# Kernel optimization log

Measured on AMD Instinct MI355X. Metric: run time of the kernel, lower is better.

## Reference

```python
import jax, jax.numpy as jnp
import numpy as np

B, N, D = 4, 8192, 128
H = 4 * D  # exp_factor * features
EPS = 1e-5


def layer_norm(x):
    # fresh nn.LayerNorm each call -> weight=1, bias=0 (no learned affine)
    mu = jnp.mean(x, axis=-1, keepdims=True)
    var = jnp.var(x, axis=-1, keepdims=True)
    return (x - mu) * jax.lax.rsqrt(var + EPS)


def setup_inputs() -> dict:
    key = jax.random.key(0)
    ks = jax.random.split(key, 8)
    x = jax.random.normal(ks[0], (B, N, D), dtype=jnp.float32)
    adj = jax.random.uniform(ks[1], (N, N), dtype=jnp.float32)
    attn_mask = jnp.ones((1,), dtype=jnp.int32)  # unused (torch masked_fill result discarded)
    pad_mask = jnp.ones((1,), dtype=jnp.int32)   # unused
    # FFN params (torch Linear default init scale ~ 1/sqrt(fan_in))
    w1 = jax.random.normal(ks[2], (D, H), dtype=jnp.float32) / np.sqrt(D)
    b1 = jnp.zeros((H,), dtype=jnp.float32)
    w2 = jax.random.normal(ks[3], (H, D), dtype=jnp.float32) / np.sqrt(H)
    b2 = jnp.zeros((D,), dtype=jnp.float32)
    return {"x": x, "adj": adj, "attn_mask": attn_mask, "pad_mask": pad_mask,
            "w1": w1, "b1": b1, "w2": w2, "b2": b2, "dim": 128}


def reference(x, adj, attn_mask, pad_mask, w1, b1, w2, b2, dim):
    # Sublayer 0: x + InrAwaSA(LN(x))
    h = layer_norm(x)                               # [B,N,D]
    # adj is provided -> scores = dense adj, shared across batch.
    # NOTE: masks are no-ops in the source (masked_fill not in-place).
    prob = jax.nn.softmax(adj, axis=-1)             # [N,N]
    attn_out = jnp.einsum('nm,bmd->bnd', prob, h)   # [B,N,D]
    x1 = x + attn_out
    # Sublayer 1: x1 + FFN(LN(x1))
    h1 = layer_norm(x1)
    ffn = jnp.maximum(h1 @ w1 + b1, 0.0) @ w2 + b2
    return x1 + ffn
```

## Files before the change

### kernel.cpp

```cpp
#include <hip/hip_runtime.h>
#include <hip/hip_bf16.h>

typedef __attribute__((ext_vector_type(8))) short bh8;
typedef __attribute__((ext_vector_type(4))) float fx4;
typedef __attribute__((ext_vector_type(8))) int i32x8;
typedef __attribute__((ext_vector_type(4))) int i32x4;

typedef const __attribute__((address_space(1))) unsigned int* gas_p;
typedef __attribute__((address_space(3))) unsigned int* las_p;

#define MFMA(a, b, c) __builtin_amdgcn_mfma_f32_16x16x32_bf16((a), (b), (c), 0, 0, 0)
#define MFMAS(a, b, c) __builtin_amdgcn_mfma_scale_f32_16x16x128_f8f6f4( \
    (a), (b), (c), 0, 0, 0, 0x7f7f7f7f, 0, 0x7f7f7f7f)

__device__ __forceinline__ unsigned short f2bf(float f) {
  unsigned u = __builtin_bit_cast(unsigned, f);
  u += 0x7fff + ((u >> 16) & 1);
  return (unsigned short)(u >> 16);
}

__device__ __forceinline__ float bflo2f(unsigned u) { return __builtin_bit_cast(float, u << 16); }

__device__ __forceinline__ void gld16(const void* g, void* l) {
  __builtin_amdgcn_global_load_lds((gas_p)g, (las_p)l, 16, 0, 0);
}

__global__ __launch_bounds__(256) void transpose_weights(const float* __restrict__ w1,
                                                         const float* __restrict__ w2,
                                                         unsigned short* __restrict__ w1t,
                                                         unsigned short* __restrict__ w2t) {
  const int tgl = blockIdx.x * 256 + threadIdx.x;
  { const int h = tgl >> 7, d = tgl & 127; w1t[tgl] = f2bf(w1[d * 512 + h]); }
  { const int d = tgl >> 9, h = tgl & 511; w2t[tgl] = f2bf(w2[h * 128 + d]); }
}

__global__ __launch_bounds__(256) void ln1_transpose(const float* __restrict__ x,
                                                     unsigned char* __restrict__ ht) {
  const int t = threadIdx.x, lane = t & 63, w = t >> 6;
  const int mt = blockIdx.x, b = blockIdx.y;
  __shared__ unsigned short tile[128 * 64];
  const float* xb = x + ((size_t)b * 8192 + (size_t)mt * 64) * 128;
  for (int it = 0; it < 16; ++it) {
    const int r = w * 16 + it;
    const float2 v = *(const float2*)(xb + r * 128 + lane * 2);
    float s = v.x + v.y, s2 = v.x * v.x + v.y * v.y;
    #pragma unroll
    for (int o = 1; o < 64; o <<= 1) { s += __shfl_xor(s, o); s2 += __shfl_xor(s2, o); }
    const float mean = s * 0.0078125f;
    const float var = s2 * 0.0078125f - mean * mean;
    const float rstd = rsqrtf(var + 1e-5f);
    const int mc = r >> 3, ml = r & 7;
    const int d0 = lane * 2, d1 = d0 + 1;
    tile[d0 * 64 + ((mc ^ (d0 & 7)) << 3) + ml] = f2bf((v.x - mean) * rstd);
    tile[d1 * 64 + ((mc ^ (d1 & 7)) << 3) + ml] = f2bf((v.y - mean) * rstd);
  }
  __syncthreads();
  unsigned char* hb = ht + (size_t)b * 128 * 8192 + (size_t)mt * 64;
  #pragma unroll
  for (int i = 0; i < 4; ++i) {
    const int idx = i * 256 + t;
    const int d = idx >> 3, mc = idx & 7;
    const bh8 vv = *(const bh8*)(tile + d * 64 + ((mc ^ (d & 7)) << 3));
    int lo = 0, hi = 0;
    lo = __builtin_amdgcn_cvt_pk_fp8_f32(bflo2f((unsigned short)vv[0]),
                                         bflo2f((unsigned short)vv[1]), lo, false);
    lo = __builtin_amdgcn_cvt_pk_fp8_f32(bflo2f((unsigned short)vv[2]),
                                         bflo2f((unsigned short)vv[3]), lo, true);
    hi = __builtin_amdgcn_cvt_pk_fp8_f32(bflo2f((unsigned short)vv[4]),
                                         bflo2f((unsigned short)vv[5]), hi, false);
    hi = __builtin_amdgcn_cvt_pk_fp8_f32(bflo2f((unsigned short)vv[6]),
                                         bflo2f((unsigned short)vv[7]), hi, true);
    *(uint2*)(hb + (size_t)d * 8192 + mc * 8) = (uint2){(unsigned)lo, (unsigned)hi};
  }
}

#define PH_SYNC { __builtin_amdgcn_sched_barrier(0); __builtin_amdgcn_s_barrier(); \
                  __builtin_amdgcn_sched_barrier(0); \
                  asm volatile("s_waitcnt lgkmcnt(0)" ::: "memory"); \
                  __builtin_amdgcn_sched_barrier(0); __builtin_amdgcn_s_setprio(1); }
#define PH_END  { __builtin_amdgcn_s_setprio(0); __builtin_amdgcn_sched_barrier(0); \
                  __builtin_amdgcn_s_barrier(); __builtin_amdgcn_sched_barrier(0); }
#define PH_END_VM0 { __builtin_amdgcn_s_setprio(0); \
                  asm volatile("s_waitcnt vmcnt(0)" ::: "memory"); \
                  __builtin_amdgcn_sched_barrier(0); __builtin_amdgcn_s_barrier(); \
                  __builtin_amdgcn_sched_barrier(0); }

__global__ __launch_bounds__(512, 2) void fused_attn(const float* __restrict__ adj,
                                                     const unsigned char* __restrict__ ht,
                                                     unsigned short* __restrict__ pbuf,
                                                     float* __restrict__ sden) {
  const int tid = threadIdx.x, lane = tid & 63, w = tid >> 6;
  const int wm = w >> 2, wn = w & 3;
  const int mt = blockIdx.x, z = blockIdx.y;
  const int kbase = z * 2048;

  __shared__ unsigned char Al[128 * 128];
  __shared__ unsigned char Bl[2][512 * 128];

  fx4 acc[4][8];
  #pragma unroll
  for (int i = 0; i < 4; ++i)
    #pragma unroll
    for (int j = 0; j < 8; ++j) acc[i][j] = (fx4){0.f, 0.f, 0.f, 0.f};

  i32x8 afr[4];

  const int ar = tid >> 2, aq = tid & 3;
  const float* aroot = adj + (size_t)(mt * 128 + ar) * 8192 + kbase;
  float sacc = 0.f;
  float4 a4[8];
  unsigned pk[8];

  auto issueAdj = [&](int tau) {
    #pragma unroll
    for (int j = 0; j < 8; ++j)
      a4[j] = *(const float4*)(aroot + tau * 128 + j * 16 + aq * 4);
  };
  auto expCvt = [&]() {
    #pragma unroll
    for (int j = 0; j < 8; ++j) {
      const float e0 = __expf(a4[j].x), e1 = __expf(a4[j].y);
      const float e2 = __expf(a4[j].z), e3 = __expf(a4[j].w);
      sacc += (e0 + e1) + (e2 + e3);
      int d = 0;
      d = __builtin_amdgcn_cvt_pk_fp8_f32(e0, e1, d, false);
      d = __builtin_amdgcn_cvt_pk_fp8_f32(e2, e3, d, true);
      pk[j] = (unsigned)d;
    }
  };
  auto writeA = [&]() {
    #pragma unroll
    for (int j = 0; j < 8; ++j)
      *(unsigned*)&Al[ar * 128 + ((j ^ (ar & 7)) << 4) + aq * 4] = pk[j];
  };
  auto stageB2 = [&](unsigned char* dst, int pp, int tau) {
    #pragma unroll
    for (int k = 0; k < 2; ++k) {
      const int cc = pp * 2 + k;
      const int row = cc * 64 + (tid >> 3), g = tid & 7;
      gld16(ht + (size_t)row * 8192 + kbase + tau * 128 + ((g ^ (row & 7)) << 4),
            dst + cc * 8192 + tid * 16);
    }
  };
  auto ldAall = [&]() {
    #pragma unroll
    for (int mf = 0; mf < 4; ++mf) {
      const int rr = wm * 64 + mf * 16 + (lane & 15);
      const int gb = (lane >> 4) * 2;
      const unsigned char* base = &Al[rr * 128];
      const i32x4 lo = *(const i32x4*)(base + ((gb ^ (rr & 7)) << 4));
      const i32x4 hi = *(const i32x4*)(base + (((gb + 1) ^ (rr & 7)) << 4));
      afr[mf] = (i32x8){lo.x, lo.y, lo.z, lo.w, hi.x, hi.y, hi.z, hi.w};
    }
  };

  issueAdj(0);
  #pragma unroll
  for (int pp = 0; pp < 4; ++pp) stageB2(Bl[0], pp, 0);
  expCvt();
  writeA();
  asm volatile("s_waitcnt lgkmcnt(0) vmcnt(0)" ::: "memory");
  __builtin_amdgcn_sched_barrier(0);
  __builtin_amdgcn_s_barrier();
  __builtin_amdgcn_sched_barrier(0);

  for (int tt = 0; tt < 16; ++tt) {
    const unsigned char* Bcur = Bl[tt & 1];
    unsigned char* Bnxt = Bl[(tt + 1) & 1];
    const bool more = (tt < 15);
    #pragma unroll
    for (int p = 0; p < 8; ++p) {
      const int c = wn * 128 + p * 16 + (lane & 15);
      const int gb = (lane >> 4) * 2;
      const unsigned char* cb = &Bcur[c * 128];
      const i32x4 blo = *(const i32x4*)(cb + ((gb ^ (c & 7)) << 4));
      const i32x4 bhi = *(const i32x4*)(cb + (((gb + 1) ^ (c & 7)) << 4));
      const i32x8 bfr = (i32x8){blo.x, blo.y, blo.z, blo.w, bhi.x, bhi.y, bhi.z, bhi.w};
      if (p == 0) { ldAall(); if (more) issueAdj(tt + 1); }
      if (p < 4 && more) stageB2(Bnxt, p, tt + 1);
      if (p == 5 && more) expCvt();
      if (p == 6 && more) writeA();
      PH_SYNC;
      #pragma unroll
      for (int mf = 0; mf < 4; ++mf)
        acc[mf][p] = MFMAS(afr[mf], bfr, acc[mf][p]);
      if (p == 7) { PH_END_VM0; } else { PH_END; }
    }
  }

  sacc += __shfl_xor(sacc, 1);
  sacc += __shfl_xor(sacc, 2);
  if (aq == 0) sden[(size_t)z * 8192 + mt * 128 + ar] = sacc;

  unsigned short* po = pbuf + (size_t)z * 8192 * 512;
  #pragma unroll
  for (int mf = 0; mf < 4; ++mf)
    #pragma unroll
    for (int nf = 0; nf < 8; ++nf) {
      const int col = wn * 128 + nf * 16 + (lane & 15);
      #pragma unroll
      for (int q = 0; q < 4; ++q) {
        const int row = mt * 128 + wm * 64 + mf * 16 + (lane >> 4) * 4 + q;
        po[(size_t)row * 512 + col] = f2bf(acc[mf][nf][q]);
      }
    }
}

#define SWZ16(ks, r) (((((ks) & 7) ^ ((r) & 7)) | ((ks) & 8)))
__global__ __launch_bounds__(512) void ln_ffn_kernel(const float* __restrict__ x,
                                                     const unsigned short* __restrict__ pbuf,
                                                     const float* __restrict__ sden,
                                                     const unsigned short* __restrict__ w1t,
                                                     const unsigned short* __restrict__ w2t,
                                                     const float* __restrict__ b1,
                                                     const float* __restrict__ b2,
                                                     float* __restrict__ out) {
  const int t = threadIdx.x, lane = t & 63, w = t >> 6;
  const int wr = w >> 1, wc = w & 1;
  const int row0 = blockIdx.x * 128;
  __shared__ unsigned short As[128 * 128];
  __shared__ unsigned short W1c[128 * 128];
  __shared__ unsigned short W2c[128 * 128];
  __shared__ unsigned short Ts[128 * 128];

  auto stageW1 = [&](int hc) {
    #pragma unroll
    for (int i = 0; i < 4; ++i) {
      const int idx = i * 512 + t;
      const int row = idx >> 4, kc = idx & 15;
      const int kcs = (kc & 8) | ((kc & 7) ^ (row & 7));
      gld16(w1t + (size_t)(hc * 128 + row) * 128 + kcs * 8, W1c + (idx & ~63) * 8);
    }
  };
  auto stageW2 = [&](int hc) {
    #pragma unroll
    for (int i = 0; i < 4; ++i) {
      const int idx = i * 512 + t;
      const int row = idx >> 4, kc = idx & 15;
      const int kcs = (kc & 8) | ((kc & 7) ^ (row & 7));
      gld16(w2t + (size_t)row * 512 + hc * 128 + kcs * 8, W2c + (idx & ~63) * 8);
    }
  };

  stageW1(0); stageW2(0);

  const int r = t >> 2, q = t & 3, c0 = q * 32;
  const int rowg = row0 + r;
  const int bb = rowg >> 13, nn = rowg & 8191;
  float xv[32];
  {
    const float den = sden[nn] + sden[8192 + nn] + sden[16384 + nn] + sden[24576 + nn];
    const float rinv = 1.f / den;
    const float* xp = x + (size_t)rowg * 128 + c0;
    #pragma unroll
    for (int j = 0; j < 8; ++j) {
      const float4 v4 = *(const float4*)(xp + 4 * j);
      xv[4 * j] = v4.x; xv[4 * j + 1] = v4.y; xv[4 * j + 2] = v4.z; xv[4 * j + 3] = v4.w;
    }
    #pragma unroll
    for (int z = 0; z < 4; ++z) {
      const unsigned short* pp = pbuf + ((size_t)z * 8192 + nn) * 512 + bb * 128 + c0;
      #pragma unroll
      for (int j = 0; j < 4; ++j) {
        const bh8 pv = *(const bh8*)(pp + 8 * j);
        #pragma unroll
        for (int e = 0; e < 8; ++e) xv[8 * j + e] += bflo2f((unsigned short)pv[e]) * rinv;
      }
    }
  }
  float s = 0.f, s2 = 0.f;
  #pragma unroll
  for (int j = 0; j < 32; ++j) { s += xv[j]; s2 += xv[j] * xv[j]; }
  s += __shfl_xor(s, 1); s2 += __shfl_xor(s2, 1);
  s += __shfl_xor(s, 2); s2 += __shfl_xor(s2, 2);
  const float mean = s * 0.0078125f;
  const float var = s2 * 0.0078125f - mean * mean;
  const float rstd = rsqrtf(var + 1e-5f);
  #pragma unroll
  for (int j = 0; j < 4; ++j) {
    const int g = q * 4 + j;
    bh8 pk;
    #pragma unroll
    for (int e = 0; e < 8; ++e) pk[e] = (short)f2bf((xv[8 * j + e] - mean) * rstd);
    *(bh8*)(As + r * 128 + SWZ16(g, r) * 8) = pk;
  }
  __syncthreads();

  fx4 accO[2][4];
  #pragma unroll
  for (int i = 0; i < 2; ++i)
    #pragma unroll
    for (int j = 0; j < 4; ++j) accO[i][j] = (fx4){0.f, 0.f, 0.f, 0.f};

  for (int hc = 0; hc < 4; ++hc) {
    if (hc > 0) stageW2(hc);
    fx4 accT[2][4];
    #pragma unroll
    for (int i = 0; i < 2; ++i)
      #pragma unroll
      for (int j = 0; j < 4; ++j) accT[i][j] = (fx4){0.f, 0.f, 0.f, 0.f};
    #pragma unroll
    for (int kk = 0; kk < 4; ++kk) {
      const int ks = kk * 4 + (lane >> 4);
      bh8 af[2], bfr[4];
      #pragma unroll
      for (int f = 0; f < 2; ++f) {
        const int ra = wr * 32 + f * 16 + (lane & 15);
        af[f] = *(const bh8*)(As + ra * 128 + SWZ16(ks, ra) * 8);
      }
      #pragma unroll
      for (int f = 0; f < 4; ++f) {
        const int rb = wc * 64 + f * 16 + (lane & 15);
        bfr[f] = *(const bh8*)(W1c + rb * 128 + SWZ16(ks, rb) * 8);
      }
      #pragma unroll
      for (int fm = 0; fm < 2; ++fm)
        #pragma unroll
        for (int fn = 0; fn < 4; ++fn) accT[fm][fn] = MFMA(af[fm], bfr[fn], accT[fm][fn]);
    }
    #pragma unroll
    for (int fm = 0; fm < 2; ++fm)
      #pragma unroll
      for (int fn = 0; fn < 4; ++fn) {
        const int col = wc * 64 + fn * 16 + (lane & 15);
        const float bv = b1[hc * 128 + col];
        const int c = col >> 3;
        #pragma unroll
        for (int qq = 0; qq < 4; ++qq) {
          const int row = wr * 32 + fm * 16 + (lane >> 4) * 4 + qq;
          float vv = accT[fm][fn][qq] + bv;
          vv = fmaxf(vv, 0.f);
          Ts[row * 128 + SWZ16(c, row) * 8 + (col & 7)] = f2bf(vv);
        }
      }
    __syncthreads();
    if (hc < 3) {
      stageW1(hc + 1);
    } else {
      float* dst = (r < 64) ? (float*)As + r * 128 + c0 : (float*)W1c + (r - 64) * 128 + c0;
      #pragma unroll
      for (int j = 0; j < 8; ++j)
        *(float4*)(dst + 4 * j) =
            (float4){xv[4 * j], xv[4 * j + 1], xv[4 * j + 2], xv[4 * j + 3]};
    }
    #pragma unroll
    for (int kk = 0; kk < 4; ++kk) {
      const int ks = kk * 4 + (lane >> 4);
      bh8 af[2], bfr[4];
      #pragma unroll
      for (int f = 0; f < 2; ++f) {
        const int ra = wr * 32 + f * 16 + (lane & 15);
        af[f] = *(const bh8*)(Ts + ra * 128 + SWZ16(ks, ra) * 8);
      }
      #pragma unroll
      for (int f = 0; f < 4; ++f) {
        const int rb = wc * 64 + f * 16 + (lane & 15);
        bfr[f] = *(const bh8*)(W2c + rb * 128 + SWZ16(ks, rb) * 8);
      }
      #pragma unroll
      for (int fm = 0; fm < 2; ++fm)
        #pragma unroll
        for (int fn = 0; fn < 4; ++fn) accO[fm][fn] = MFMA(af[fm], bfr[fn], accO[fm][fn]);
    }
    __syncthreads();
  }

  const float* x1a = (const float*)As;
  const float* x1b = (const float*)W1c;
  float* op = out + (size_t)row0 * 128;
  #pragma unroll
  for (int fm = 0; fm < 2; ++fm)
    #pragma unroll
    for (int fn = 0; fn < 4; ++fn) {
      const int col = wc * 64 + fn * 16 + (lane & 15);
      const float bv = b2[col];
      #pragma unroll
      for (int qq = 0; qq < 4; ++qq) {
        const int row = wr * 32 + fm * 16 + (lane >> 4) * 4 + qq;
        const float x1v = (row < 64) ? x1a[row * 128 + col] : x1b[(row - 64) * 128 + col];
        op[row * 128 + col] = x1v + accO[fm][fn][qq] + bv;
      }
    }
}

extern "C" void kernel_launch(void* const* d_in, const int* in_sizes, int n_in,
                              void* d_out, int out_size, void* d_ws, size_t ws_size,
                              hipStream_t stream) {
  const float* x   = (const float*)d_in[0];
  const float* adj = (const float*)d_in[1];
  const float* w1  = (const float*)d_in[4];
  const float* b1  = (const float*)d_in[5];
  const float* w2  = (const float*)d_in[6];
  const float* b2  = (const float*)d_in[7];
  float* out = (float*)d_out;

  char* p = (char*)d_ws;
  unsigned short* w1t  = (unsigned short*)p; p += (size_t)512 * 128 * 2;
  unsigned short* w2t  = (unsigned short*)p; p += (size_t)128 * 512 * 2;
  unsigned char*  ht   = (unsigned char*)p;  p += (size_t)4 * 128 * 8192;
  unsigned short* pbuf = (unsigned short*)p; p += (size_t)4 * 8192 * 512 * 2;
  float*          sden = (float*)p;          p += (size_t)4 * 8192 * 4;

  transpose_weights<<<256, 256, 0, stream>>>(w1, w2, w1t, w2t);
  ln1_transpose<<<dim3(128, 4), 256, 0, stream>>>(x, ht);
  fused_attn<<<dim3(64, 4), 512, 0, stream>>>(adj, ht, pbuf, sden);
  ln_ffn_kernel<<<256, 512, 0, stream>>>(x, pbuf, sden, w1t, w2t, b1, b2, out);
}
```

Measured before the change: 151.5 us.

## Drop LDS staging of B tiles; load fp8 B fragments directly from global

The attention GEMM kernel now loads the fp8 h^T fragments straight from global memory into registers instead of staging them through double-buffered LDS with async global_load_lds. Blocks shrink to 256 threads covering 64 rows, with twice as many blocks, and the fine-grained per-MFMA barrier and priority phases are replaced by a simple per-k-step barrier. This removes the LDS capacity and barrier overhead and raises occupancy. In exchange each block re-reads B from global or L2 with no LDS reuse and no explicit prefetch overlap, so B traffic doubles and exposed load latency may rise.

```diff
diff --git a/kernel.cpp b/kernel.cpp
--- a/kernel.cpp
+++ b/kernel.cpp
@@ -74,28 +74,15 @@
   }
 }
 
-#define PH_SYNC { __builtin_amdgcn_sched_barrier(0); __builtin_amdgcn_s_barrier(); \
-                  __builtin_amdgcn_sched_barrier(0); \
-                  asm volatile("s_waitcnt lgkmcnt(0)" ::: "memory"); \
-                  __builtin_amdgcn_sched_barrier(0); __builtin_amdgcn_s_setprio(1); }
-#define PH_END  { __builtin_amdgcn_s_setprio(0); __builtin_amdgcn_sched_barrier(0); \
-                  __builtin_amdgcn_s_barrier(); __builtin_amdgcn_sched_barrier(0); }
-#define PH_END_VM0 { __builtin_amdgcn_s_setprio(0); \
-                  asm volatile("s_waitcnt vmcnt(0)" ::: "memory"); \
-                  __builtin_amdgcn_sched_barrier(0); __builtin_amdgcn_s_barrier(); \
-                  __builtin_amdgcn_sched_barrier(0); }
-
-__global__ __launch_bounds__(512, 2) void fused_attn(const float* __restrict__ adj,
+__global__ __launch_bounds__(256, 2) void fused_attn(const float* __restrict__ adj,
                                                      const unsigned char* __restrict__ ht,
                                                      unsigned short* __restrict__ pbuf,
                                                      float* __restrict__ sden) {
-  const int tid = threadIdx.x, lane = tid & 63, w = tid >> 6;
-  const int wm = w >> 2, wn = w & 3;
+  const int tid = threadIdx.x, lane = tid & 63, wn = tid >> 6;
   const int mt = blockIdx.x, z = blockIdx.y;
   const int kbase = z * 2048;
 
-  __shared__ unsigned char Al[128 * 128];
-  __shared__ unsigned char Bl[2][512 * 128];
+  __shared__ unsigned char Al[64 * 128];
 
   fx4 acc[4][8];
   #pragma unroll
@@ -106,7 +93,7 @@
   i32x8 afr[4];
 
   const int ar = tid >> 2, aq = tid & 3;
-  const float* aroot = adj + (size_t)(mt * 128 + ar) * 8192 + kbase;
+  const float* aroot = adj + (size_t)(mt * 64 + ar) * 8192 + kbase;
   float sacc = 0.f;
   float4 a4[8];
   unsigned pk[8];
@@ -133,19 +120,10 @@
     for (int j = 0; j < 8; ++j)
       *(unsigned*)&Al[ar * 128 + ((j ^ (ar & 7)) << 4) + aq * 4] = pk[j];
   };
-  auto stageB2 = [&](unsigned char* dst, int pp, int tau) {
-    #pragma unroll
-    for (int k = 0; k < 2; ++k) {
-      const int cc = pp * 2 + k;
-      const int row = cc * 64 + (tid >> 3), g = tid & 7;
-      gld16(ht + (size_t)row * 8192 + kbase + tau * 128 + ((g ^ (row & 7)) << 4),
-            dst + cc * 8192 + tid * 16);
-    }
-  };
   auto ldAall = [&]() {
     #pragma unroll
     for (int mf = 0; mf < 4; ++mf) {
-      const int rr = wm * 64 + mf * 16 + (lane & 15);
+      const int rr = mf * 16 + (lane & 15);
       const int gb = (lane >> 4) * 2;
       const unsigned char* base = &Al[rr * 128];
       const i32x4 lo = *(const i32x4*)(base + ((gb ^ (rr & 7)) << 4));
@@ -155,42 +133,47 @@
   };
 
   issueAdj(0);
-  #pragma unroll
-  for (int pp = 0; pp < 4; ++pp) stageB2(Bl[0], pp, 0);
   expCvt();
   writeA();
-  asm volatile("s_waitcnt lgkmcnt(0) vmcnt(0)" ::: "memory");
+  asm volatile("s_waitcnt lgkmcnt(0)" ::: "memory");
   __builtin_amdgcn_sched_barrier(0);
   __builtin_amdgcn_s_barrier();
   __builtin_amdgcn_sched_barrier(0);
 
   for (int tt = 0; tt < 16; ++tt) {
-    const unsigned char* Bcur = Bl[tt & 1];
-    unsigned char* Bnxt = Bl[(tt + 1) & 1];
-    const bool more = (tt < 15);
+    ldAall();
+    if (tt < 15) issueAdj(tt + 1);
+    asm volatile("s_waitcnt lgkmcnt(0)" ::: "memory");
+    __builtin_amdgcn_sched_barrier(0);
+    __builtin_amdgcn_s_barrier();
+    __builtin_amdgcn_sched_barrier(0);
+
+    const unsigned char* bb = ht + kbase + tt * 128 + (size_t)(lane >> 4) * 32;
     #pragma unroll
     for (int p = 0; p < 8; ++p) {
       const int c = wn * 128 + p * 16 + (lane & 15);
-      const int gb = (lane >> 4) * 2;
-      const unsigned char* cb = &Bcur[c * 128];
-      const i32x4 blo = *(const i32x4*)(cb + ((gb ^ (c & 7)) << 4));
-      const i32x4 bhi = *(const i32x4*)(cb + (((gb + 1) ^ (c & 7)) << 4));
+      const unsigned char* cb = bb + (size_t)c * 8192;
+      const i32x4 blo = *(const i32x4*)(cb);
+      const i32x4 bhi = *(const i32x4*)(cb + 16);
       const i32x8 bfr = (i32x8){blo.x, blo.y, blo.z, blo.w, bhi.x, bhi.y, bhi.z, bhi.w};
-      if (p == 0) { ldAall(); if (more) issueAdj(tt + 1); }
-      if (p < 4 && more) stageB2(Bnxt, p, tt + 1);
-      if (p == 5 && more) expCvt();
-      if (p == 6 && more) writeA();
-      PH_SYNC;
       #pragma unroll
       for (int mf = 0; mf < 4; ++mf)
         acc[mf][p] = MFMAS(afr[mf], bfr, acc[mf][p]);
-      if (p == 7) { PH_END_VM0; } else { PH_END; }
-    }
+    }
+
+    if (tt < 15) {
+      expCvt();
+      writeA();
+      asm volatile("s_waitcnt lgkmcnt(0)" ::: "memory");
+      __builtin_amdgcn_sched_barrier(0);
+    }
+    __builtin_amdgcn_s_barrier();
+    __builtin_amdgcn_sched_barrier(0);
   }
 
   sacc += __shfl_xor(sacc, 1);
   sacc += __shfl_xor(sacc, 2);
-  if (aq == 0) sden[(size_t)z * 8192 + mt * 128 + ar] = sacc;
+  if (aq == 0) sden[(size_t)z * 8192 + mt * 64 + ar] = sacc;
 
   unsigned short* po = pbuf + (size_t)z * 8192 * 512;
   #pragma unroll
@@ -200,7 +183,7 @@
       const int col = wn * 128 + nf * 16 + (lane & 15);
       #pragma unroll
       for (int q = 0; q < 4; ++q) {
-        const int row = mt * 128 + wm * 64 + mf * 16 + (lane >> 4) * 4 + q;
+        const int row = mt * 64 + mf * 16 + (lane >> 4) * 4 + q;
         po[(size_t)row * 512 + col] = f2bf(acc[mf][nf][q]);
       }
     }
@@ -403,6 +386,6 @@
 
   transpose_weights<<<256, 256, 0, stream>>>(w1, w2, w1t, w2t);
   ln1_transpose<<<dim3(128, 4), 256, 0, stream>>>(x, ht);
-  fused_attn<<<dim3(64, 4), 512, 0, stream>>>(adj, ht, pbuf, sden);
+  fused_attn<<<dim3(128, 4), 256, 0, stream>>>(adj, ht, pbuf, sden);
   ln_ffn_kernel<<<256, 512, 0, stream>>>(x, pbuf, sden, w1t, w2t, b1, b2, out);
 }
```

Result: slower. 180.4 us (+19.1%).
